# Kernel optimization log

Measured on AMD Instinct MI355X. Metric: run time of the kernel, lower is better.

The kernel has to match this reference:

```python
import jax, jax.numpy as jnp
import numpy as np
import math

B, S, HID = 2, 2048, 2048
H, KVH, D = 16, 4, 128
EPS = 1e-6
THETA = 10000.0


def _rope_tables(key):
    inv_freq = 1.0 / (THETA ** (jnp.arange(0, D, 2, dtype=jnp.float32) / D))  # [D/2]
    pos = jnp.arange(S, dtype=jnp.float32)
    freqs = pos[:, None] * inv_freq[None, :]            # [S, D/2]
    emb = jnp.concatenate([freqs, freqs], axis=-1)      # [S, D]
    cos = jnp.broadcast_to(jnp.cos(emb)[None], (B, S, D))
    sin = jnp.broadcast_to(jnp.sin(emb)[None], (B, S, D))
    return cos, sin


def setup_inputs() -> dict:
    key = jax.random.key(0)
    ks = jax.random.split(key, 6)
    hidden_states = jax.random.normal(ks[0], (B, S, HID), dtype=jnp.float32)
    # causal additive mask, broadcastable to [B, H, S, S]
    causal = jnp.tril(jnp.ones((S, S), dtype=jnp.bool_))
    attention_mask = jnp.where(causal, 0.0, jnp.finfo(jnp.float32).min)[None, None]
    cos, sin = _rope_tables(key)
    sc = 0.02
    Wq = jax.random.normal(ks[1], (HID, H * D), dtype=jnp.float32) * sc
    Wk = jax.random.normal(ks[2], (HID, KVH * D), dtype=jnp.float32) * sc
    Wv = jax.random.normal(ks[3], (HID, KVH * D), dtype=jnp.float32) * sc
    Wo = jax.random.normal(ks[4], (H * D, HID), dtype=jnp.float32) * sc
    q_norm_w = jnp.ones((D,), dtype=jnp.float32)
    k_norm_w = jnp.ones((D,), dtype=jnp.float32)
    return dict(hidden_states=hidden_states, attention_mask=attention_mask,
                cos=cos, sin=sin, Wq=Wq, Wk=Wk, Wv=Wv, Wo=Wo,
                q_norm_w=q_norm_w, k_norm_w=k_norm_w)


def _rms_norm(x, w, eps=EPS):
    dt = x.dtype
    xf = x.astype(jnp.float32)
    var = jnp.mean(xf * xf, axis=-1, keepdims=True)
    return (w * (xf * jax.lax.rsqrt(var + eps)).astype(dt)).astype(dt)


def _rotate_half(x):
    x1, x2 = jnp.split(x, 2, axis=-1)
    return jnp.concatenate([-x2, x1], axis=-1)


def reference(hidden_states, attention_mask, cos, sin, Wq, Wk, Wv, Wo, q_norm_w, k_norm_w):
    b, s, _ = hidden_states.shape
    q = (hidden_states @ Wq).reshape(b, s, H, D)
    k = (hidden_states @ Wk).reshape(b, s, KVH, D)
    v = (hidden_states @ Wv).reshape(b, s, KVH, D)
    q = _rms_norm(q, q_norm_w).transpose(0, 2, 1, 3)   # [B,H,S,D]
    k = _rms_norm(k, k_norm_w).transpose(0, 2, 1, 3)   # [B,KVH,S,D]
    v = v.transpose(0, 2, 1, 3)
    # RoPE: cos/sin [B,S,D] -> unsqueeze head dim
    c = cos[:, None]
    sn = sin[:, None]
    q = q * c + _rotate_half(q) * sn
    k = k * c + _rotate_half(k) * sn
    # repeat_kv for GQA
    n_rep = H // KVH
    k = jnp.repeat(k, n_rep, axis=1)
    v = jnp.repeat(v, n_rep, axis=1)
    scores = jnp.einsum('bhqd,bhkd->bhqk', q, k) / math.sqrt(D)
    scores = scores + attention_mask
    attn = jax.nn.softmax(scores.astype(jnp.float32), axis=-1).astype(q.dtype)
    out = jnp.einsum('bhqk,bhkd->bhqd', attn, v)
    out = out.transpose(0, 2, 1, 3).reshape(b, s, H * D)
    return out @ Wo
```

## Files before the change

### kernel.cpp

```cpp
#include <hip/hip_runtime.h>
#include <math.h>

#define B_ 2
#define S_ 2048
#define HID_ 2048
#define H_ 16
#define KVH_ 4
#define D_ 128

typedef __bf16 bf16x8 __attribute__((ext_vector_type(8)));
typedef float f32x4 __attribute__((ext_vector_type(4)));

__device__ __forceinline__ unsigned short f2bf(float x) {
  union { float f; unsigned u; } cv;
  cv.f = x;
  unsigned u = cv.u;
  u += 0x7FFFu + ((u >> 16) & 1u);
  return (unsigned short)(u >> 16);
}

__device__ __forceinline__ void gload_lds16(const unsigned short* g,
                                            unsigned short* l) {
  __builtin_amdgcn_global_load_lds(
      (const __attribute__((address_space(1))) unsigned int*)g,
      (__attribute__((address_space(3))) unsigned int*)l, 16, 0, 0);
}

__global__ __launch_bounds__(256) void convert_bf16_kernel(
    const float* __restrict__ in, unsigned short* __restrict__ out) {
  const size_t i = ((size_t)blockIdx.x * 256 + threadIdx.x) * 8;
  const float4 v0 = *reinterpret_cast<const float4*>(&in[i]);
  const float4 v1 = *reinterpret_cast<const float4*>(&in[i + 4]);
  ushort4 o0, o1;
  o0.x = f2bf(v0.x); o0.y = f2bf(v0.y); o0.z = f2bf(v0.z); o0.w = f2bf(v0.w);
  o1.x = f2bf(v1.x); o1.y = f2bf(v1.y); o1.z = f2bf(v1.z); o1.w = f2bf(v1.w);
  *reinterpret_cast<ushort4*>(&out[i]) = o0;
  *reinterpret_cast<ushort4*>(&out[i + 4]) = o1;
}

__global__ __launch_bounds__(256) void transpose_w_kernel(
    const float* __restrict__ Wq, const float* __restrict__ Wk,
    const float* __restrict__ Wv, const float* __restrict__ Wo,
    unsigned short* __restrict__ WqT, unsigned short* __restrict__ WkT,
    unsigned short* __restrict__ WvT, unsigned short* __restrict__ WoT) {
  int blk = blockIdx.x;
  const float* src;
  unsigned short* dst;
  int N;
  if (blk < 4096)      { src = Wq; dst = WqT; N = 2048; }
  else if (blk < 5120) { src = Wk; dst = WkT; N = 512;  blk -= 4096; }
  else if (blk < 6144) { src = Wv; dst = WvT; N = 512;  blk -= 5120; }
  else                 { src = Wo; dst = WoT; N = 2048; blk -= 6144; }
  const int tiles_n = N >> 5;
  const int ti = blk / tiles_n;
  const int tj = blk % tiles_n;

  __shared__ unsigned short T[32][40];
  const int t = threadIdx.x;
  const int r = t >> 3;
  const int c4 = (t & 7) * 4;

  const float4 v = *reinterpret_cast<const float4*>(
      &src[(size_t)(ti * 32 + r) * N + tj * 32 + c4]);
  T[r][c4 + 0] = f2bf(v.x);
  T[r][c4 + 1] = f2bf(v.y);
  T[r][c4 + 2] = f2bf(v.z);
  T[r][c4 + 3] = f2bf(v.w);
  __syncthreads();

  ushort4 o;
  o.x = T[c4 + 0][r];
  o.y = T[c4 + 1][r];
  o.z = T[c4 + 2][r];
  o.w = T[c4 + 3][r];
  *reinterpret_cast<ushort4*>(&dst[(size_t)(tj * 32 + r) * 2048 + ti * 32 + c4]) = o;
}

template <int MODE>
__device__ __forceinline__ void mfma_gemm_body(
    const unsigned short* __restrict__ A, const unsigned short* __restrict__ BT,
    float* __restrict__ C, int M, int N, int K, int NH, int bx, int by) {
  __shared__ unsigned short As[128 * 32];
  __shared__ unsigned short Bs[128 * 32];

  const int tid = threadIdx.x;
  const int m0 = by * 128, n0 = bx * 128;
  const int lane = tid & 63;
  const int wave = tid >> 6;
  const int wm = (wave >> 1) * 64;
  const int wn = (wave & 1) * 64;
  const int lr = lane & 15;
  const int lg = lane >> 4;

  const int sgrow = wave * 32 + (lane >> 2);
  const int sgcol = (lane & 3) * 8;
  const unsigned short* gA0 = A + (size_t)(m0 + sgrow) * K + sgcol;
  const unsigned short* gA1 = A + (size_t)(m0 + sgrow + 16) * K + sgcol;
  const unsigned short* gB0 = BT + (size_t)(n0 + sgrow) * K + sgcol;
  const unsigned short* gB1 = BT + (size_t)(n0 + sgrow + 16) * K + sgcol;
  unsigned short* lA0 = As + (size_t)(wave * 32) * 32;
  unsigned short* lA1 = As + (size_t)(wave * 32 + 16) * 32;
  unsigned short* lB0 = Bs + (size_t)(wave * 32) * 32;
  unsigned short* lB1 = Bs + (size_t)(wave * 32 + 16) * 32;

  f32x4 acc[4][4];
#pragma unroll
  for (int i = 0; i < 4; ++i)
#pragma unroll
    for (int j = 0; j < 4; ++j)
#pragma unroll
      for (int r = 0; r < 4; ++r) acc[i][j][r] = 0.0f;

  for (int k0 = 0; k0 < K; k0 += 32) {
    __syncthreads();
    gload_lds16(gA0 + k0, lA0);
    gload_lds16(gA1 + k0, lA1);
    gload_lds16(gB0 + k0, lB0);
    gload_lds16(gB1 + k0, lB1);
    __syncthreads();

    bf16x8 af[4], bfr[4];
#pragma unroll
    for (int i = 0; i < 4; ++i) {
      af[i] = *reinterpret_cast<const bf16x8*>(&As[(wm + i * 16 + lr) * 32 + lg * 8]);
      bfr[i] = *reinterpret_cast<const bf16x8*>(&Bs[(wn + i * 16 + lr) * 32 + lg * 8]);
    }
#pragma unroll
    for (int i = 0; i < 4; ++i)
#pragma unroll
      for (int j = 0; j < 4; ++j)
        acc[i][j] = __builtin_amdgcn_mfma_f32_16x16x32_bf16(
            af[i], bfr[j], acc[i][j], 0, 0, 0);
  }

#pragma unroll
  for (int i = 0; i < 4; ++i) {
#pragma unroll
    for (int j = 0; j < 4; ++j) {
#pragma unroll
      for (int r = 0; r < 4; ++r) {
        const int m = m0 + wm + i * 16 + lg * 4 + r;
        const int n = n0 + wn + j * 16 + lr;
        const float val = acc[i][j][r];
        if (MODE == 0) {
          C[(size_t)m * N + n] = val;
        } else {
          const int b = m >> 11, s = m & (S_ - 1);
          const int h = n >> 7, d = n & 127;
          const size_t idx = (((size_t)b * NH + h) * S_ + s) * D_ + d;
          if (MODE == 1) {
            C[idx] = val;
          } else {
            reinterpret_cast<unsigned short*>(C)[idx] = f2bf(val);
          }
        }
      }
    }
  }
}

__global__ __launch_bounds__(256) void qkv_gemm_kernel(
    const unsigned short* __restrict__ hsb, const unsigned short* __restrict__ WqT,
    const unsigned short* __restrict__ WkT, const unsigned short* __restrict__ WvT,
    float* __restrict__ q, float* __restrict__ k, unsigned short* __restrict__ vb) {
  const int blk = blockIdx.x;
  if (blk < 512) {
    mfma_gemm_body<1>(hsb, WqT, q, B_ * S_, H_ * D_, HID_, H_, blk & 15, blk >> 4);
  } else if (blk < 640) {
    const int t = blk - 512;
    mfma_gemm_body<1>(hsb, WkT, k, B_ * S_, KVH_ * D_, HID_, KVH_, t & 3, t >> 2);
  } else {
    const int t = blk - 640;
    mfma_gemm_body<2>(hsb, WvT, reinterpret_cast<float*>(vb),
                      B_ * S_, KVH_ * D_, HID_, KVH_, t & 3, t >> 2);
  }
}

__global__ __launch_bounds__(256) void out_gemm_kernel(
    const unsigned short* __restrict__ A, const unsigned short* __restrict__ BT,
    float* __restrict__ C) {
  mfma_gemm_body<0>(A, BT, C, B_ * S_, HID_, H_ * D_, 0, blockIdx.x, blockIdx.y);
}

__global__ __launch_bounds__(256) void norm_rope_kernel(
    const float* __restrict__ q, const float* __restrict__ k,
    unsigned short* __restrict__ qb, unsigned short* __restrict__ kb,
    const float* __restrict__ cosb, const float* __restrict__ sinb,
    const float* __restrict__ qw, const float* __restrict__ kw) {
  const int wave = threadIdx.x >> 6;
  const int lane = threadIdx.x & 63;
  const int row = blockIdx.x * 4 + wave;
  const int rows_q = B_ * S_ * H_;

  const float* p;
  unsigned short* po;
  const float* w;
  int b, s;
  if (row < rows_q) {
    p = q + (size_t)row * D_;
    po = qb + (size_t)row * D_;
    w = qw;
    b = row / (H_ * S_);
    s = row & (S_ - 1);
  } else {
    const int r = row - rows_q;
    p = k + (size_t)r * D_;
    po = kb + (size_t)r * D_;
    w = kw;
    b = r / (KVH_ * S_);
    s = r & (S_ - 1);
  }

  const float x1 = p[lane];
  const float x2 = p[lane + 64];
  float ss = x1 * x1 + x2 * x2;
#pragma unroll
  for (int off = 32; off; off >>= 1) ss += __shfl_xor(ss, off, 64);
  const float inv = rsqrtf(ss * (1.0f / D_) + 1e-6f);
  const float xn1 = x1 * inv * w[lane];
  const float xn2 = x2 * inv * w[lane + 64];

  const size_t cb = ((size_t)b * S_ + s) * D_;
  const float c1 = cosb[cb + lane], c2 = cosb[cb + lane + 64];
  const float s1 = sinb[cb + lane], s2 = sinb[cb + lane + 64];
  po[lane]      = f2bf(xn1 * c1 - xn2 * s1);
  po[lane + 64] = f2bf(xn2 * c2 + xn1 * s2);
}

__global__ __launch_bounds__(256, 2) void attn_mfma_kernel(
    const unsigned short* __restrict__ qb, const unsigned short* __restrict__ kb,
    const unsigned short* __restrict__ vb, unsigned short* __restrict__ aob) {
  const int p = blockIdx.x;
  int u, bh;
  if (p < 256) { u = p & 15; bh = p >> 4; }
  else { const int pq = p - 256; u = 15 - (pq & 15); bh = 16 + (pq >> 4); }
  const int qta = u;
  const int qtb = 31 - u;
  const int b = bh >> 4;
  const int h = bh & 15;
  const int kvh = h >> 2;

  const int tid = threadIdx.x;
  const int wv = tid >> 6;
  const int lane = tid & 63;
  const int lr = lane & 15;
  const int kg = lane >> 4;

  __shared__ unsigned short Ks[64 * 128];
  __shared__ unsigned short VT[128 * 64];
  __shared__ unsigned short PsA[64 * 64];
  __shared__ unsigned short PsB[64 * 64];

  const unsigned short* qbaseA =
      qb + (((size_t)b * H_ + h) * S_ + (size_t)qta * 64) * D_;
  const unsigned short* qbaseB =
      qb + (((size_t)b * H_ + h) * S_ + (size_t)qtb * 64) * D_;
  const unsigned short* kbase = kb + (((size_t)b * KVH_ + kvh) * S_) * D_;
  const unsigned short* vbase = vb + (((size_t)b * KVH_ + kvh) * S_) * D_;

  bf16x8 qfa[4], qfb[4];
#pragma unroll
  for (int ks = 0; ks < 4; ++ks) {
    qfa[ks] = *reinterpret_cast<const bf16x8*>(
        qbaseA + (size_t)(wv * 16 + lr) * D_ + ks * 32 + kg * 8);
    qfb[ks] = *reinterpret_cast<const bf16x8*>(
        qbaseB + (size_t)(wv * 16 + lr) * D_ + ks * 32 + kg * 8);
  }

  f32x4 oa[8], ob[8];
#pragma unroll
  for (int d0 = 0; d0 < 8; ++d0)
#pragma unroll
    for (int r = 0; r < 4; ++r) { oa[d0][r] = 0.0f; ob[d0][r] = 0.0f; }
  float ma[4] = {-1e30f, -1e30f, -1e30f, -1e30f};
  float la[4] = {0.0f, 0.0f, 0.0f, 0.0f};
  float mb[4] = {-1e30f, -1e30f, -1e30f, -1e30f};
  float lb[4] = {0.0f, 0.0f, 0.0f, 0.0f};
  const float scale = 0.08838834764831845f;

  const int krow = tid >> 4;
  const int kc8 = (tid & 15) * 8;
  const int vjp = tid & 31;
  const int vd4b = tid >> 5;

  uint4 kr[4];
  ushort4 vr0[4], vr1[4];

#pragma unroll
  for (int it = 0; it < 4; ++it) {
    kr[it] = *reinterpret_cast<const uint4*>(
        kbase + (size_t)(it * 16 + krow) * D_ + kc8);
    const int d4 = (it * 8 + vd4b) * 4;
    vr0[it] = *reinterpret_cast<const ushort4*>(
        vbase + (size_t)(2 * vjp) * D_ + d4);
    vr1[it] = *reinterpret_cast<const ushort4*>(
        vbase + (size_t)(2 * vjp + 1) * D_ + d4);
  }

  const int last = qtb;

  auto compute_tile = [&](const bf16x8* qf, f32x4* o, float* m_run,
                          float* l_run, int qtile, int kt,
                          unsigned short* Ps) {
    f32x4 s[4];
#pragma unroll
    for (int j = 0; j < 4; ++j)
#pragma unroll
      for (int r = 0; r < 4; ++r) s[j][r] = 0.0f;
    __builtin_amdgcn_s_setprio(1);
#pragma unroll
    for (int ks = 0; ks < 4; ++ks) {
#pragma unroll
      for (int j = 0; j < 4; ++j) {
        const int krw = j * 16 + lr;
        const bf16x8 kf = *reinterpret_cast<const bf16x8*>(
            &Ks[krw * 128 + ((ks * 32 + kg * 8) ^ ((krw & 7) * 8))]);
        s[j] = __builtin_amdgcn_mfma_f32_16x16x32_bf16(qf[ks], kf, s[j], 0, 0, 0);
      }
    }
    __builtin_amdgcn_s_setprio(0);

    if (kt == qtile) {
      const int qrow0 = wv * 16 + kg * 4;
#pragma unroll
      for (int j = 0; j < 4; ++j) {
        const int kcol = j * 16 + lr;
#pragma unroll
        for (int r = 0; r < 4; ++r)
          s[j][r] = (kcol <= qrow0 + r) ? s[j][r] * scale : -1e30f;
      }
    } else {
#pragma unroll
      for (int j = 0; j < 4; ++j)
#pragma unroll
        for (int r = 0; r < 4; ++r) s[j][r] *= scale;
    }

#pragma unroll
    for (int r = 0; r < 4; ++r) {
      float mx = fmaxf(fmaxf(s[0][r], s[1][r]), fmaxf(s[2][r], s[3][r]));
      mx = fmaxf(mx, __shfl_xor(mx, 1));
      mx = fmaxf(mx, __shfl_xor(mx, 2));
      mx = fmaxf(mx, __shfl_xor(mx, 4));
      mx = fmaxf(mx, __shfl_xor(mx, 8));
      const float mn = fmaxf(m_run[r], mx);
      const float al = __expf(m_run[r] - mn);
      float sum = 0.0f;
#pragma unroll
      for (int j = 0; j < 4; ++j) {
        s[j][r] = __expf(s[j][r] - mn);
        sum += s[j][r];
      }
      sum += __shfl_xor(sum, 1);
      sum += __shfl_xor(sum, 2);
      sum += __shfl_xor(sum, 4);
      sum += __shfl_xor(sum, 8);
      l_run[r] = l_run[r] * al + sum;
      m_run[r] = mn;
#pragma unroll
      for (int d0 = 0; d0 < 8; ++d0) o[d0][r] *= al;
    }

#pragma unroll
    for (int r = 0; r < 4; ++r) {
      const int prow = wv * 16 + kg * 4 + r;
      const int swz = (prow & 7) * 8;
#pragma unroll
      for (int j = 0; j < 4; ++j)
        Ps[prow * 64 + ((j * 16 + lr) ^ swz)] = f2bf(s[j][r]);
    }

    __builtin_amdgcn_s_setprio(1);
#pragma unroll
    for (int ks = 0; ks < 2; ++ks) {
      const int arow = wv * 16 + lr;
      const bf16x8 pf = *reinterpret_cast<const bf16x8*>(
          &Ps[arow * 64 + ((ks * 32 + kg * 8) ^ ((arow & 7) * 8))]);
#pragma unroll
      for (int d0 = 0; d0 < 8; ++d0) {
        const int vrow = d0 * 16 + lr;
        const bf16x8 vf = *reinterpret_cast<const bf16x8*>(
            &VT[vrow * 64 + ((ks * 32 + kg * 8) ^ ((vrow & 7) * 8))]);
        o[d0] = __builtin_amdgcn_mfma_f32_16x16x32_bf16(pf, vf, o[d0], 0, 0, 0);
      }
    }
    __builtin_amdgcn_s_setprio(0);
  };

  for (int kt = 0; kt <= last; ++kt) {
#pragma unroll
    for (int it = 0; it < 4; ++it) {
      const int r = it * 16 + krow;
      *reinterpret_cast<uint4*>(&Ks[r * 128 + (kc8 ^ ((r & 7) * 8))]) = kr[it];
      const int d4 = (it * 8 + vd4b) * 4;
      const int rsw = 2 * vjp;
      ushort2 w0, w1, w2, w3;
      w0.x = vr0[it].x; w0.y = vr1[it].x;
      w1.x = vr0[it].y; w1.y = vr1[it].y;
      w2.x = vr0[it].z; w2.y = vr1[it].z;
      w3.x = vr0[it].w; w3.y = vr1[it].w;
      *reinterpret_cast<ushort2*>(&VT[(d4 + 0) * 64 + (rsw ^ (((d4 + 0) & 7) * 8))]) = w0;
      *reinterpret_cast<ushort2*>(&VT[(d4 + 1) * 64 + (rsw ^ (((d4 + 1) & 7) * 8))]) = w1;
      *reinterpret_cast<ushort2*>(&VT[(d4 + 2) * 64 + (rsw ^ (((d4 + 2) & 7) * 8))]) = w2;
      *reinterpret_cast<ushort2*>(&VT[(d4 + 3) * 64 + (rsw ^ (((d4 + 3) & 7) * 8))]) = w3;
    }
    __syncthreads();

    if (kt < last) {
      const size_t koff = (size_t)(kt + 1) * 64;
#pragma unroll
      for (int it = 0; it < 4; ++it) {
        kr[it] = *reinterpret_cast<const uint4*>(
            kbase + (koff + it * 16 + krow) * D_ + kc8);
        const int d4 = (it * 8 + vd4b) * 4;
        vr0[it] = *reinterpret_cast<const ushort4*>(
            vbase + (koff + 2 * vjp) * D_ + d4);
        vr1[it] = *reinterpret_cast<const ushort4*>(
            vbase + (koff + 2 * vjp + 1) * D_ + d4);
      }
    }

    if (kt <= qta) compute_tile(qfa, oa, ma, la, qta, kt, PsA);
    compute_tile(qfb, ob, mb, lb, qtb, kt, PsB);
    __syncthreads();
  }

#pragma unroll
  for (int r = 0; r < 4; ++r) {
    const float inva = 1.0f / la[r];
    const float invb = 1.0f / lb[r];
    const size_t rowa = (size_t)b * S_ + (size_t)qta * 64 + wv * 16 + kg * 4 + r;
    const size_t rowb = (size_t)b * S_ + (size_t)qtb * 64 + wv * 16 + kg * 4 + r;
    unsigned short* opa = aob + rowa * (H_ * D_) + h * D_;
    unsigned short* opb = aob + rowb * (H_ * D_) + h * D_;
#pragma unroll
    for (int d0 = 0; d0 < 8; ++d0) {
      opa[d0 * 16 + lr] = f2bf(oa[d0][r] * inva);
      opb[d0 * 16 + lr] = f2bf(ob[d0][r] * invb);
    }
  }
}

extern "C" void kernel_launch(void* const* d_in, const int* in_sizes, int n_in,
                              void* d_out, int out_size, void* d_ws, size_t ws_size,
                              hipStream_t stream) {
  const float* hs   = (const float*)d_in[0];
  const float* cosb = (const float*)d_in[2];
  const float* sinb = (const float*)d_in[3];
  const float* Wq   = (const float*)d_in[4];
  const float* Wk   = (const float*)d_in[5];
  const float* Wv   = (const float*)d_in[6];
  const float* Wo   = (const float*)d_in[7];
  const float* qw   = (const float*)d_in[8];
  const float* kw   = (const float*)d_in[9];

  char* ws = (char*)d_ws;
  float* q  = (float*)ws;                     ws += (size_t)8388608 * 4;
  float* k  = (float*)ws;                     ws += (size_t)2097152 * 4;
  unsigned short* qbb = (unsigned short*)ws;  ws += (size_t)8388608 * 2;
  unsigned short* kbb = (unsigned short*)ws;  ws += (size_t)2097152 * 2;
  unsigned short* vbb = (unsigned short*)ws;  ws += (size_t)2097152 * 2;
  unsigned short* hsb = (unsigned short*)ws;  ws += (size_t)8388608 * 2;
  unsigned short* WqT = (unsigned short*)ws;  ws += (size_t)4194304 * 2;
  unsigned short* WkT = (unsigned short*)ws;  ws += (size_t)1048576 * 2;
  unsigned short* WvT = (unsigned short*)ws;  ws += (size_t)1048576 * 2;
  unsigned short* WoT = (unsigned short*)ws;  ws += (size_t)4194304 * 2;
  unsigned short* aob = (unsigned short*)ws;  ws += (size_t)8388608 * 2;
  float* out = (float*)d_out;

  const dim3 blk(256);

  convert_bf16_kernel<<<dim3(4096), blk, 0, stream>>>(hs, hsb);
  transpose_w_kernel<<<dim3(10240), blk, 0, stream>>>(
      Wq, Wk, Wv, Wo, WqT, WkT, WvT, WoT);

  qkv_gemm_kernel<<<dim3(768), blk, 0, stream>>>(hsb, WqT, WkT, WvT, q, k, vbb);

  norm_rope_kernel<<<dim3((B_ * S_ * (H_ + KVH_)) / 4), blk, 0, stream>>>(
      q, k, qbb, kbb, cosb, sinb, qw, kw);

  attn_mfma_kernel<<<dim3(512), blk, 0, stream>>>(qbb, kbb, vbb, aob);

  out_gemm_kernel<<<dim3(HID_ / 128, (B_ * S_) / 128), blk, 0, stream>>>(
      aob, WoT, out);
}
```

Before: 424.7 us.

## Fuse QK RMSNorm and RoPE into QKV GEMM epilogue; lazy softmax rescale

The GEMM warp tiling changes from 2x2 waves of 64x64 to 4 waves of 32x128, so each wave holds full 128-wide head rows. That lets the Q/K projection epilogue do RMSNorm and RoPE in registers and write bf16 directly, which removes the fp32 q/k intermediates and the separate norm_rope kernel. The attention kernel now uses exp2 with a pre-scaled log2e factor and skips rescaling the running max and output when the row max grows by at most a threshold. It also merges the two P shared buffers into one. The wider B-fragment load per wave raises register pressure, and the lazy rescale risks overflow-related accuracy issues if the threshold logic is wrong.

```diff
diff --git a/kernel.cpp b/kernel.cpp
--- a/kernel.cpp
+++ b/kernel.cpp
@@ -79,7 +79,9 @@
 template <int MODE>
 __device__ __forceinline__ void mfma_gemm_body(
     const unsigned short* __restrict__ A, const unsigned short* __restrict__ BT,
-    float* __restrict__ C, int M, int N, int K, int NH, int bx, int by) {
+    float* __restrict__ C, int M, int N, int K, int NH, int bx, int by,
+    const float* __restrict__ cosb, const float* __restrict__ sinb,
+    const float* __restrict__ nw) {
   __shared__ unsigned short As[128 * 32];
   __shared__ unsigned short Bs[128 * 32];
 
@@ -87,10 +89,9 @@
   const int m0 = by * 128, n0 = bx * 128;
   const int lane = tid & 63;
   const int wave = tid >> 6;
-  const int wm = (wave >> 1) * 64;
-  const int wn = (wave & 1) * 64;
+  const int wm = wave * 32;
   const int lr = lane & 15;
-  const int lg = lane >> 4;
+  const int kg = lane >> 4;
 
   const int sgrow = wave * 32 + (lane >> 2);
   const int sgcol = (lane & 3) * 8;
@@ -103,11 +104,11 @@
   unsigned short* lB0 = Bs + (size_t)(wave * 32) * 32;
   unsigned short* lB1 = Bs + (size_t)(wave * 32 + 16) * 32;
 
-  f32x4 acc[4][4];
-#pragma unroll
-  for (int i = 0; i < 4; ++i)
-#pragma unroll
-    for (int j = 0; j < 4; ++j)
+  f32x4 acc[2][8];
+#pragma unroll
+  for (int i = 0; i < 2; ++i)
+#pragma unroll
+    for (int j = 0; j < 8; ++j)
 #pragma unroll
       for (int r = 0; r < 4; ++r) acc[i][j][r] = 0.0f;
 
@@ -119,40 +120,76 @@
     gload_lds16(gB1 + k0, lB1);
     __syncthreads();
 
-    bf16x8 af[4], bfr[4];
-#pragma unroll
-    for (int i = 0; i < 4; ++i) {
-      af[i] = *reinterpret_cast<const bf16x8*>(&As[(wm + i * 16 + lr) * 32 + lg * 8]);
-      bfr[i] = *reinterpret_cast<const bf16x8*>(&Bs[(wn + i * 16 + lr) * 32 + lg * 8]);
-    }
-#pragma unroll
-    for (int i = 0; i < 4; ++i)
-#pragma unroll
-      for (int j = 0; j < 4; ++j)
+    bf16x8 af[2], bfr[8];
+#pragma unroll
+    for (int i = 0; i < 2; ++i)
+      af[i] = *reinterpret_cast<const bf16x8*>(&As[(wm + i * 16 + lr) * 32 + kg * 8]);
+#pragma unroll
+    for (int j = 0; j < 8; ++j)
+      bfr[j] = *reinterpret_cast<const bf16x8*>(&Bs[(j * 16 + lr) * 32 + kg * 8]);
+#pragma unroll
+    for (int i = 0; i < 2; ++i)
+#pragma unroll
+      for (int j = 0; j < 8; ++j)
         acc[i][j] = __builtin_amdgcn_mfma_f32_16x16x32_bf16(
             af[i], bfr[j], acc[i][j], 0, 0, 0);
   }
 
-#pragma unroll
-  for (int i = 0; i < 4; ++i) {
-#pragma unroll
-    for (int j = 0; j < 4; ++j) {
+  if (MODE == 0) {
+#pragma unroll
+    for (int i = 0; i < 2; ++i)
 #pragma unroll
       for (int r = 0; r < 4; ++r) {
-        const int m = m0 + wm + i * 16 + lg * 4 + r;
-        const int n = n0 + wn + j * 16 + lr;
-        const float val = acc[i][j][r];
-        if (MODE == 0) {
-          C[(size_t)m * N + n] = val;
-        } else {
-          const int b = m >> 11, s = m & (S_ - 1);
-          const int h = n >> 7, d = n & 127;
-          const size_t idx = (((size_t)b * NH + h) * S_ + s) * D_ + d;
-          if (MODE == 1) {
-            C[idx] = val;
-          } else {
-            reinterpret_cast<unsigned short*>(C)[idx] = f2bf(val);
-          }
+        const int m = m0 + wm + i * 16 + kg * 4 + r;
+        float* row = C + (size_t)m * N + n0;
+#pragma unroll
+        for (int j = 0; j < 8; ++j) row[j * 16 + lr] = acc[i][j][r];
+      }
+  } else if (MODE == 2) {
+    const int h = n0 >> 7;
+#pragma unroll
+    for (int i = 0; i < 2; ++i)
+#pragma unroll
+      for (int r = 0; r < 4; ++r) {
+        const int m = m0 + wm + i * 16 + kg * 4 + r;
+        const int bb = m >> 11, s = m & (S_ - 1);
+        unsigned short* row = reinterpret_cast<unsigned short*>(C) +
+                              (((size_t)bb * NH + h) * S_ + s) * D_;
+#pragma unroll
+        for (int j = 0; j < 8; ++j) row[j * 16 + lr] = f2bf(acc[i][j][r]);
+      }
+  } else {
+    float wreg[8];
+#pragma unroll
+    for (int j = 0; j < 8; ++j) wreg[j] = nw[j * 16 + lr];
+    const int h = n0 >> 7;
+#pragma unroll
+    for (int i = 0; i < 2; ++i) {
+#pragma unroll
+      for (int r = 0; r < 4; ++r) {
+        const int m = m0 + wm + i * 16 + kg * 4 + r;
+        const int bb = m >> 11, s = m & (S_ - 1);
+        float ssum = 0.0f;
+#pragma unroll
+        for (int j = 0; j < 8; ++j) ssum += acc[i][j][r] * acc[i][j][r];
+        ssum += __shfl_xor(ssum, 1);
+        ssum += __shfl_xor(ssum, 2);
+        ssum += __shfl_xor(ssum, 4);
+        ssum += __shfl_xor(ssum, 8);
+        const float inv = rsqrtf(ssum * (1.0f / 128.0f) + 1e-6f);
+        float xn[8];
+#pragma unroll
+        for (int j = 0; j < 8; ++j) xn[j] = acc[i][j][r] * inv * wreg[j];
+        const size_t cb = ((size_t)bb * S_ + s) * D_;
+        unsigned short* row = reinterpret_cast<unsigned short*>(C) +
+                              (((size_t)bb * NH + h) * S_ + s) * D_;
+#pragma unroll
+        for (int j = 0; j < 4; ++j) {
+          const int d = j * 16 + lr;
+          const float c = cosb[cb + d];
+          const float sn = sinb[cb + d];
+          row[d]      = f2bf(xn[j] * c - xn[j + 4] * sn);
+          row[d + 64] = f2bf(xn[j + 4] * c + xn[j] * sn);
         }
       }
     }
@@ -162,69 +199,33 @@
 __global__ __launch_bounds__(256) void qkv_gemm_kernel(
     const unsigned short* __restrict__ hsb, const unsigned short* __restrict__ WqT,
     const unsigned short* __restrict__ WkT, const unsigned short* __restrict__ WvT,
-    float* __restrict__ q, float* __restrict__ k, unsigned short* __restrict__ vb) {
+    unsigned short* __restrict__ qb, unsigned short* __restrict__ kb,
+    unsigned short* __restrict__ vb,
+    const float* __restrict__ cosb, const float* __restrict__ sinb,
+    const float* __restrict__ qw, const float* __restrict__ kw) {
   const int blk = blockIdx.x;
   if (blk < 512) {
-    mfma_gemm_body<1>(hsb, WqT, q, B_ * S_, H_ * D_, HID_, H_, blk & 15, blk >> 4);
+    mfma_gemm_body<3>(hsb, WqT, reinterpret_cast<float*>(qb),
+                      B_ * S_, H_ * D_, HID_, H_, blk & 15, blk >> 4,
+                      cosb, sinb, qw);
   } else if (blk < 640) {
     const int t = blk - 512;
-    mfma_gemm_body<1>(hsb, WkT, k, B_ * S_, KVH_ * D_, HID_, KVH_, t & 3, t >> 2);
+    mfma_gemm_body<3>(hsb, WkT, reinterpret_cast<float*>(kb),
+                      B_ * S_, KVH_ * D_, HID_, KVH_, t & 3, t >> 2,
+                      cosb, sinb, kw);
   } else {
     const int t = blk - 640;
     mfma_gemm_body<2>(hsb, WvT, reinterpret_cast<float*>(vb),
-                      B_ * S_, KVH_ * D_, HID_, KVH_, t & 3, t >> 2);
+                      B_ * S_, KVH_ * D_, HID_, KVH_, t & 3, t >> 2,
+                      nullptr, nullptr, nullptr);
   }
 }
 
 __global__ __launch_bounds__(256) void out_gemm_kernel(
     const unsigned short* __restrict__ A, const unsigned short* __restrict__ BT,
     float* __restrict__ C) {
-  mfma_gemm_body<0>(A, BT, C, B_ * S_, HID_, H_ * D_, 0, blockIdx.x, blockIdx.y);
-}
-
-__global__ __launch_bounds__(256) void norm_rope_kernel(
-    const float* __restrict__ q, const float* __restrict__ k,
-    unsigned short* __restrict__ qb, unsigned short* __restrict__ kb,
-    const float* __restrict__ cosb, const float* __restrict__ sinb,
-    const float* __restrict__ qw, const float* __restrict__ kw) {
-  const int wave = threadIdx.x >> 6;
-  const int lane = threadIdx.x & 63;
-  const int row = blockIdx.x * 4 + wave;
-  const int rows_q = B_ * S_ * H_;
-
-  const float* p;
-  unsigned short* po;
-  const float* w;
-  int b, s;
-  if (row < rows_q) {
-    p = q + (size_t)row * D_;
-    po = qb + (size_t)row * D_;
-    w = qw;
-    b = row / (H_ * S_);
-    s = row & (S_ - 1);
-  } else {
-    const int r = row - rows_q;
-    p = k + (size_t)r * D_;
-    po = kb + (size_t)r * D_;
-    w = kw;
-    b = r / (KVH_ * S_);
-    s = r & (S_ - 1);
-  }
-
-  const float x1 = p[lane];
-  const float x2 = p[lane + 64];
-  float ss = x1 * x1 + x2 * x2;
-#pragma unroll
-  for (int off = 32; off; off >>= 1) ss += __shfl_xor(ss, off, 64);
-  const float inv = rsqrtf(ss * (1.0f / D_) + 1e-6f);
-  const float xn1 = x1 * inv * w[lane];
-  const float xn2 = x2 * inv * w[lane + 64];
-
-  const size_t cb = ((size_t)b * S_ + s) * D_;
-  const float c1 = cosb[cb + lane], c2 = cosb[cb + lane + 64];
-  const float s1 = sinb[cb + lane], s2 = sinb[cb + lane + 64];
-  po[lane]      = f2bf(xn1 * c1 - xn2 * s1);
-  po[lane + 64] = f2bf(xn2 * c2 + xn1 * s2);
+  mfma_gemm_body<0>(A, BT, C, B_ * S_, HID_, H_ * D_, 0, blockIdx.x, blockIdx.y,
+                    nullptr, nullptr, nullptr);
 }
 
 __global__ __launch_bounds__(256, 2) void attn_mfma_kernel(
@@ -248,8 +249,7 @@
 
   __shared__ unsigned short Ks[64 * 128];
   __shared__ unsigned short VT[128 * 64];
-  __shared__ unsigned short PsA[64 * 64];
-  __shared__ unsigned short PsB[64 * 64];
+  __shared__ unsigned short Ps[64 * 64];
 
   const unsigned short* qbaseA =
       qb + (((size_t)b * H_ + h) * S_ + (size_t)qta * 64) * D_;
@@ -276,7 +276,8 @@
   float la[4] = {0.0f, 0.0f, 0.0f, 0.0f};
   float mb[4] = {-1e30f, -1e30f, -1e30f, -1e30f};
   float lb[4] = {0.0f, 0.0f, 0.0f, 0.0f};
-  const float scale = 0.08838834764831845f;
+  const float scl2 = 0.08838834764831845f * 1.4426950408889634f;
+  const float THR = 11.0f;
 
   const int krow = tid >> 4;
   const int kc8 = (tid & 15) * 8;
@@ -300,8 +301,7 @@
   const int last = qtb;
 
   auto compute_tile = [&](const bf16x8* qf, f32x4* o, float* m_run,
-                          float* l_run, int qtile, int kt,
-                          unsigned short* Ps) {
+                          float* l_run, int qtile, int kt) {
     f32x4 s[4];
 #pragma unroll
     for (int j = 0; j < 4; ++j)
@@ -327,15 +327,17 @@
         const int kcol = j * 16 + lr;
 #pragma unroll
         for (int r = 0; r < 4; ++r)
-          s[j][r] = (kcol <= qrow0 + r) ? s[j][r] * scale : -1e30f;
+          s[j][r] = (kcol <= qrow0 + r) ? s[j][r] * scl2 : -1e30f;
       }
     } else {
 #pragma unroll
       for (int j = 0; j < 4; ++j)
 #pragma unroll
-        for (int r = 0; r < 4; ++r) s[j][r] *= scale;
-    }
-
+        for (int r = 0; r < 4; ++r) s[j][r] *= scl2;
+    }
+
+    float mx4[4];
+    float grow = -1e30f;
 #pragma unroll
     for (int r = 0; r < 4; ++r) {
       float mx = fmaxf(fmaxf(s[0][r], s[1][r]), fmaxf(s[2][r], s[3][r]));
@@ -343,22 +345,44 @@
       mx = fmaxf(mx, __shfl_xor(mx, 2));
       mx = fmaxf(mx, __shfl_xor(mx, 4));
       mx = fmaxf(mx, __shfl_xor(mx, 8));
-      const float mn = fmaxf(m_run[r], mx);
-      const float al = __expf(m_run[r] - mn);
-      float sum = 0.0f;
-#pragma unroll
-      for (int j = 0; j < 4; ++j) {
-        s[j][r] = __expf(s[j][r] - mn);
-        sum += s[j][r];
-      }
-      sum += __shfl_xor(sum, 1);
-      sum += __shfl_xor(sum, 2);
-      sum += __shfl_xor(sum, 4);
-      sum += __shfl_xor(sum, 8);
-      l_run[r] = l_run[r] * al + sum;
-      m_run[r] = mn;
-#pragma unroll
-      for (int d0 = 0; d0 < 8; ++d0) o[d0][r] *= al;
+      mx4[r] = mx;
+      grow = fmaxf(grow, mx - m_run[r]);
+    }
+    if (__all(grow <= THR)) {
+#pragma unroll
+      for (int r = 0; r < 4; ++r) {
+        float sum = 0.0f;
+#pragma unroll
+        for (int j = 0; j < 4; ++j) {
+          s[j][r] = exp2f(s[j][r] - m_run[r]);
+          sum += s[j][r];
+        }
+        sum += __shfl_xor(sum, 1);
+        sum += __shfl_xor(sum, 2);
+        sum += __shfl_xor(sum, 4);
+        sum += __shfl_xor(sum, 8);
+        l_run[r] += sum;
+      }
+    } else {
+#pragma unroll
+      for (int r = 0; r < 4; ++r) {
+        const float mn = fmaxf(m_run[r], mx4[r]);
+        const float al = exp2f(m_run[r] - mn);
+        float sum = 0.0f;
+#pragma unroll
+        for (int j = 0; j < 4; ++j) {
+          s[j][r] = exp2f(s[j][r] - mn);
+          sum += s[j][r];
+        }
+        sum += __shfl_xor(sum, 1);
+        sum += __shfl_xor(sum, 2);
+        sum += __shfl_xor(sum, 4);
+        sum += __shfl_xor(sum, 8);
+        l_run[r] = l_run[r] * al + sum;
+        m_run[r] = mn;
+#pragma unroll
+        for (int d0 = 0; d0 < 8; ++d0) o[d0][r] *= al;
+      }
     }
 
 #pragma unroll
@@ -420,8 +444,8 @@
       }
     }
 
-    if (kt <= qta) compute_tile(qfa, oa, ma, la, qta, kt, PsA);
-    compute_tile(qfb, ob, mb, lb, qtb, kt, PsB);
+    if (kt <= qta) compute_tile(qfa, oa, ma, la, qta, kt);
+    compute_tile(qfb, ob, mb, lb, qtb, kt);
     __syncthreads();
   }
 
@@ -455,8 +479,6 @@
   const float* kw   = (const float*)d_in[9];
 
   char* ws = (char*)d_ws;
-  float* q  = (float*)ws;                     ws += (size_t)8388608 * 4;
-  float* k  = (float*)ws;                     ws += (size_t)2097152 * 4;
   unsigned short* qbb = (unsigned short*)ws;  ws += (size_t)8388608 * 2;
   unsigned short* kbb = (unsigned short*)ws;  ws += (size_t)2097152 * 2;
   unsigned short* vbb = (unsigned short*)ws;  ws += (size_t)2097152 * 2;
@@ -474,10 +496,8 @@
   transpose_w_kernel<<<dim3(10240), blk, 0, stream>>>(
       Wq, Wk, Wv, Wo, WqT, WkT, WvT, WoT);
 
-  qkv_gemm_kernel<<<dim3(768), blk, 0, stream>>>(hsb, WqT, WkT, WvT, q, k, vbb);
-
-  norm_rope_kernel<<<dim3((B_ * S_ * (H_ + KVH_)) / 4), blk, 0, stream>>>(
-      q, k, qbb, kbb, cosb, sinb, qw, kw);
+  qkv_gemm_kernel<<<dim3(768), blk, 0, stream>>>(
+      hsb, WqT, WkT, WvT, qbb, kbb, vbb, cosb, sinb, qw, kw);
 
   attn_mfma_kernel<<<dim3(512), blk, 0, stream>>>(qbb, kbb, vbb, aob);
 
```

Result: no change. 420.2 us (-1.1%).
